# Kernel tuning notes

Hardware: AMD Instinct MI355X
Metric: run time of the kernel (lower is better)

Reference implementation:

```python
import jax, jax.numpy as jnp
import numpy as np

B, T, F = 8192, 50, 24
H1, LAT, H3 = 64, 32, 64  # encoder LSTM1, bottleneck LSTM2, decoder LSTM3


def lstm(x, W, U, b, return_sequences):
    """Keras LSTM with activation='relu', recurrent_activation='sigmoid'.
    x: [B, T, D]; W: [D, 4H]; U: [H, 4H]; b: [4H]. Gate order: i, f, g(c), o.
    """
    H = U.shape[0]
    xW = jnp.einsum('btd,dh->bth', x, W) + b          # precompute input projections
    xW_t = jnp.swapaxes(xW, 0, 1)                     # [T, B, 4H]
    h0 = jnp.zeros((x.shape[0], H), x.dtype)
    c0 = jnp.zeros((x.shape[0], H), x.dtype)

    def step(carry, xt):
        h, c = carry
        z = xt + h @ U                                 # [B, 4H]
        i = jax.nn.sigmoid(z[:, 0 * H:1 * H])
        f = jax.nn.sigmoid(z[:, 1 * H:2 * H])
        g = jax.nn.relu(z[:, 2 * H:3 * H])             # activation='relu'
        o = jax.nn.sigmoid(z[:, 3 * H:4 * H])
        c_new = f * c + i * g
        h_new = o * jax.nn.relu(c_new)                 # activation='relu'
        return (h_new, c_new), h_new

    (h_T, _), hs = jax.lax.scan(step, (h0, c0), xW_t)
    if return_sequences:
        return jnp.swapaxes(hs, 0, 1)                  # [B, T, H]
    return h_T                                         # [B, H]


def setup_inputs() -> dict:
    key = jax.random.key(0)
    ks = jax.random.split(key, 12)
    s = 0.05
    return {
        'x':  jax.random.normal(ks[0], (B, T, F), jnp.float32),
        'W1': jax.random.normal(ks[1], (F, 4 * H1), jnp.float32) * s,
        'U1': jax.random.normal(ks[2], (H1, 4 * H1), jnp.float32) * s,
        'b1': jnp.zeros((4 * H1,), jnp.float32),
        'W2': jax.random.normal(ks[3], (H1, 4 * LAT), jnp.float32) * s,
        'U2': jax.random.normal(ks[4], (LAT, 4 * LAT), jnp.float32) * s,
        'b2': jnp.zeros((4 * LAT,), jnp.float32),
        'W3': jax.random.normal(ks[5], (LAT, 4 * H3), jnp.float32) * s,
        'U3': jax.random.normal(ks[6], (H3, 4 * H3), jnp.float32) * s,
        'b3': jnp.zeros((4 * H3,), jnp.float32),
        'Wd': jax.random.normal(ks[7], (H3, F), jnp.float32) * s,
        'bd': jnp.zeros((F,), jnp.float32),
    }


def reference(x, W1, U1, b1, W2, U2, b2, W3, U3, b3, Wd, bd):
    # Encoder
    h1 = lstm(x, W1, U1, b1, return_sequences=True)    # [B, T, 64]
    z = lstm(h1, W2, U2, b2, return_sequences=False)   # [B, latent]
    # Decoder
    zr = jnp.broadcast_to(z[:, None, :], (z.shape[0], T, z.shape[1]))  # RepeatVector
    h3 = lstm(zr, W3, U3, b3, return_sequences=True)   # [B, T, 64]
    out = jnp.einsum('bth,hf->btf', h3, Wd) + bd       # TimeDistributed Dense
    return out
```

## Files before the change

### kernel.cpp

```cpp
#include <hip/hip_runtime.h>
#include <cstdint>

#define BB 8192
#define TT 50
#define FF 24
#define ROWS 32
#define LOG2E 1.4426950408889634f

typedef __attribute__((ext_vector_type(8))) short short8;
typedef __attribute__((ext_vector_type(4))) float f32x4;

__device__ __forceinline__ float sig2(float xs){
  return __builtin_amdgcn_rcpf(1.0f + exp2f(-xs));
}

__device__ __forceinline__ unsigned short rne16(float v){
  unsigned b = __float_as_uint(v);
  b += 0x7FFFu + ((b >> 16) & 1u);
  return (unsigned short)(b >> 16);
}

__device__ __forceinline__ unsigned pack2(float a, float b){
  unsigned ua = __float_as_uint(a); ua += 0x7FFFu + ((ua >> 16) & 1u);
  unsigned ub = __float_as_uint(b); ub += 0x7FFFu + ((ub >> 16) & 1u);
  return (ua >> 16) | (ub & 0xFFFF0000u);
}

__device__ __forceinline__ void phase_barrier(){
  __builtin_amdgcn_sched_barrier(0);
  asm volatile("s_waitcnt lgkmcnt(0)" ::: "memory");
  __builtin_amdgcn_s_barrier();
  asm volatile("" ::: "memory");
  __builtin_amdgcn_sched_barrier(0);
}

#define MFMA(A,B,C) __builtin_amdgcn_mfma_f32_16x16x32_bf16((A),(B),(C),0,0,0)


__global__ __launch_bounds__(1024,4)
void ae_fused(
    const float* __restrict__ x,
    const float* __restrict__ W1, const float* __restrict__ U1, const float* __restrict__ b1,
    const float* __restrict__ W2, const float* __restrict__ U2, const float* __restrict__ b2,
    const float* __restrict__ W3, const float* __restrict__ U3, const float* __restrict__ b3,
    const float* __restrict__ Wd, const float* __restrict__ bd,
    float* __restrict__ out)
{
  constexpr int AS1 = 104, AS2 = 40, AS3 = 72;
  __shared__ __align__(16) unsigned short a1[2][ROWS*AS1];
  __shared__ __align__(16) unsigned short a2[2][ROWS*AS2];
  __shared__ __align__(16) unsigned short a3[2][ROWS*AS3];

  const int tid = threadIdx.x, wave = tid>>6, lane = tid&63;
  const int quad = lane>>4, li = lane&15;
  const int w7 = wave&7, rg = wave>>3;
  const int b0 = blockIdx.x*ROWS;
  const int arow = rg*16 + li;

  const int gl = li & 3;
  const float scl = (gl==2) ? 1.0f : LOG2E;

  short8 A1w[2][3];
  f32x4 bi1[2];
#pragma unroll
  for (int tp=0; tp<2; ++tp){
    const int zc = gl*64 + 8*w7 + 2*(li>>2) + tp;
#pragma unroll
    for (int ks=0; ks<3; ++ks){
      short8 v1;
#pragma unroll
      for (int j=0; j<8; ++j){
        const int kk = quad*8 + j;
        float w;
        if (ks < 2) w = U1[(ks*32+kk)*256+zc];
        else        w = (kk<24) ? W1[kk*256+zc] : 0.f;
        v1[j] = (short)rne16(w*scl);
      }
      A1w[tp][ks]=v1;
    }
#pragma unroll
    for (int i2=0;i2<4;++i2)
      bi1[tp][i2] = b1[i2*64 + 8*w7 + 2*quad + tp] * ((i2==2)?1.0f:LOG2E);
  }
  short8 A1w2[3];
  f32x4 bi2;
  {
    const int zc = gl*32 + 4*w7 + (li>>2);
#pragma unroll
    for (int ks=0; ks<3; ++ks){
      short8 v1;
#pragma unroll
      for (int j=0; j<8; ++j){
        const int kk = quad*8 + j;
        float w = (ks<2) ? W2[(ks*32+kk)*128+zc] : U2[kk*128+zc];
        v1[j] = (short)rne16(w*scl);
      }
      A1w2[ks]=v1;
    }
#pragma unroll
    for (int i2=0;i2<4;++i2)
      bi2[i2] = b2[i2*32 + 4*w7 + quad] * ((i2==2)?1.0f:LOG2E);
  }

  { unsigned* p1 = (unsigned*)a1; for (int i=tid;i<2*ROWS*AS1/2;i+=1024) p1[i]=0u;
    unsigned* p2 = (unsigned*)a2; for (int i=tid;i<2*ROWS*AS2/2;i+=1024) p2[i]=0u;
    unsigned* p3 = (unsigned*)a3; for (int i=tid;i<2*ROWS*AS3/2;i+=1024) p3[i]=0u; }
  __syncthreads();
  if (tid < ROWS*FF){
    const int r = tid/FF, f = tid - r*FF;
    a1[0][r*AS1 + 64 + f] = rne16(x[((size_t)(b0+r)*TT + 0)*FF + f]);
  }
  int pr=0, pf=0; const float* xp=nullptr;
  float va=0.f, vb=0.f;
  const bool st = (tid < ROWS*FF);
  if (st){
    pr = tid/FF; pf = tid - pr*FF;
    xp = x + (size_t)(b0+pr)*TT*FF + pf;
    va = xp[1*FF];
    vb = xp[2*FF];
  }
  float c1s[2] = {0.f,0.f};
  float c2s = 0.f;
  const int rb1 = arow*AS1;
  const int rb2 = arow*AS2;
  const int hw1p = rb1 + 8*w7 + 2*quad;
  const int hw2 = rb2 + 4*w7 + quad;
  __syncthreads();

#pragma unroll 1
  for (int t=0; t<=TT; ++t){
    const int s = t&1, ns = s^1;
    float vc = 0.f;
    if (st && t+3 < TT) vc = xp[(t+3)*FF];
    short8 Bh0 = *(const short8*)&a1[s][rb1 +      quad*8];
    short8 Bh1 = *(const short8*)&a1[s][rb1 + 32 + quad*8];
    if (t < TT){
      short8 Bx = *(const short8*)&a1[s][rb1 + 64 + quad*8];
      float hp[2];
#pragma unroll
      for (int tp=0; tp<2; ++tp){
        f32x4 C = bi1[tp];
        C = MFMA(A1w[tp][0], Bh0, C);
        C = MFMA(A1w[tp][1], Bh1, C);
        C = MFMA(A1w[tp][2], Bx,  C);
        const float ig = sig2(C[0]), fg = sig2(C[1]);
        const float gg = fmaxf(C[2],0.f), og = sig2(C[3]);
        const float cn = fg*c1s[tp] + ig*gg; c1s[tp] = cn;
        hp[tp] = og*fmaxf(cn,0.f);
      }
      *(unsigned*)&a1[ns][hw1p] = pack2(hp[0], hp[1]);
    }
    if (t >= 1){
      f32x4 C = bi2;
      C = MFMA(A1w2[0], Bh0, C);
      C = MFMA(A1w2[1], Bh1, C);
      {
        short8 Bh2 = *(const short8*)&a2[s][rb2 + quad*8];
        C = MFMA(A1w2[2], Bh2, C);
      }
      const float ig = sig2(C[0]), fg = sig2(C[1]);
      const float gg = fmaxf(C[2],0.f), og = sig2(C[3]);
      const float cn = fg*c2s + ig*gg; c2s = cn;
      const float h = og*fmaxf(cn,0.f);
      a2[ns][hw2] = rne16(h);
    }
    if (st && t < TT-1){
      a1[ns][pr*AS1 + 64 + pf] = rne16(va);
      va = vb; vb = vc;
    }
    phase_barrier();
  }

  short8 A1u[2][2];
  short8 A1w3[2];
  f32x4 bi3[2];
#pragma unroll
  for (int tp=0; tp<2; ++tp){
    const int zc = gl*64 + 8*w7 + 2*(li>>2) + tp;
#pragma unroll
    for (int ks=0; ks<2; ++ks){
      short8 v1;
#pragma unroll
      for (int j=0; j<8; ++j){
        const int k = ks*32 + quad*8 + j;
        v1[j] = (short)rne16(U3[k*256+zc]*scl);
      }
      A1u[tp][ks]=v1;
    }
    {
      short8 v1;
#pragma unroll
      for (int j=0; j<8; ++j){
        const int k = quad*8 + j;
        v1[j] = (short)rne16(W3[k*256+zc]*scl);
      }
      A1w3[tp]=v1;
    }
#pragma unroll
    for (int i2=0;i2<4;++i2)
      bi3[tp][i2] = b3[i2*64 + 8*w7 + 2*quad + tp] * ((i2==2)?1.0f:LOG2E);
  }
  const bool dW = (w7 < 2);
  const int dcol = w7*16 + li;
  const bool dOK = dW && (dcol < 24);
  const float bdv = dOK ? bd[dcol] : 0.f;
  short8 Bd1[2];
  if (dW){
#pragma unroll
    for (int ks=0; ks<2; ++ks){
      short8 v1;
#pragma unroll
      for (int j=0; j<8; ++j){
        const int k = ks*32 + quad*8 + j;
        v1[j] = (short)rne16(dOK ? Wd[k*24+dcol] : 0.f);
      }
      Bd1[ks]=v1;
    }
  }

  f32x4 zr[2];
  {
    short8 Ba = *(const short8*)&a2[1][rb2 + quad*8];
#pragma unroll
    for (int tp=0; tp<2; ++tp){
      f32x4 C = bi3[tp];
      C = MFMA(A1w3[tp], Ba, C);
      zr[tp] = C;
    }
  }
  float c3s[2] = {0.f,0.f};
  const int rb3 = arow*AS3;
  const int hw3p = rb3 + 8*w7 + 2*quad;

#pragma unroll 1
  for (int t=0; t<=TT; ++t){
    const int s = t&1, ns = s^1;
    if (t < TT){
      short8 Ba[2];
#pragma unroll
      for (int ks=0; ks<2; ++ks)
        Ba[ks] = *(const short8*)&a3[s][rb3 + ks*32 + quad*8];
      float hp[2];
#pragma unroll
      for (int tp=0; tp<2; ++tp){
        f32x4 C = zr[tp];
        C = MFMA(A1u[tp][0], Ba[0], C);
        C = MFMA(A1u[tp][1], Ba[1], C);
        const float ig = sig2(C[0]), fg = sig2(C[1]);
        const float gg = fmaxf(C[2],0.f), og = sig2(C[3]);
        const float cn = fg*c3s[tp] + ig*gg; c3s[tp] = cn;
        hp[tp] = og*fmaxf(cn,0.f);
      }
      *(unsigned*)&a3[ns][hw3p] = pack2(hp[0], hp[1]);
      if (dW && t > 0){
        f32x4 Cd = {bdv,bdv,bdv,bdv};
        Cd = MFMA(Ba[0], Bd1[0], Cd);
        Cd = MFMA(Ba[1], Bd1[1], Cd);
        if (dcol < 24){
#pragma unroll
          for (int i2=0;i2<4;++i2)
            out[((size_t)(b0+rg*16+quad*4+i2)*TT + (t-1))*FF + dcol] = Cd[i2];
        }
      }
    } else {
      if (dW){
        f32x4 Cd = {bdv,bdv,bdv,bdv};
#pragma unroll
        for (int ks=0; ks<2; ++ks){
          short8 Ba = *(const short8*)&a3[s][rb3 + ks*32 + quad*8];
          Cd = MFMA(Ba, Bd1[ks], Cd);
        }
        if (dcol < 24){
#pragma unroll
          for (int i2=0;i2<4;++i2)
            out[((size_t)(b0+rg*16+quad*4+i2)*TT + (TT-1))*FF + dcol] = Cd[i2];
        }
      }
    }
    phase_barrier();
  }
}

extern "C" void kernel_launch(void* const* d_in, const int* in_sizes, int n_in,
                              void* d_out, int out_size, void* d_ws, size_t ws_size,
                              hipStream_t stream){
  const float* x  = (const float*)d_in[0];
  const float* W1 = (const float*)d_in[1];
  const float* U1 = (const float*)d_in[2];
  const float* b1 = (const float*)d_in[3];
  const float* W2 = (const float*)d_in[4];
  const float* U2 = (const float*)d_in[5];
  const float* b2 = (const float*)d_in[6];
  const float* W3 = (const float*)d_in[7];
  const float* U3 = (const float*)d_in[8];
  const float* b3 = (const float*)d_in[9];
  const float* Wd = (const float*)d_in[10];
  const float* bd = (const float*)d_in[11];
  float* out = (float*)d_out;

  hipLaunchKernelGGL(ae_fused, dim3(BB/ROWS), dim3(1024), 0, stream,
                     x, W1, U1, b1, W2, U2, b2, W3, U3, b3, Wd, bd, out);
}
```

Before: 219.9 us.

## Halve rows per block and spread gate columns across all sixteen waves

Each block now handles 16 batch rows instead of 32. The 16 waves each own one gate-column tile for layers 1 and 3 instead of two, and only waves 8-15 compute the layer-2 LSTM. The goal is a shorter per-step serial chain per wave (half the MFMAs and activations) and twice as many blocks, with launch bounds raised to 8 blocks per CU. The cost is half the rows per weight load, idle waves on layer 2, and higher register and occupancy pressure.

```diff
diff --git a/kernel.cpp b/kernel.cpp
--- a/kernel.cpp
+++ b/kernel.cpp
@@ -4,7 +4,7 @@
 #define BB 8192
 #define TT 50
 #define FF 24
-#define ROWS 32
+#define ROWS 16
 #define LOG2E 1.4426950408889634f
 
 typedef __attribute__((ext_vector_type(8))) short short8;
@@ -18,12 +18,6 @@
   unsigned b = __float_as_uint(v);
   b += 0x7FFFu + ((b >> 16) & 1u);
   return (unsigned short)(b >> 16);
-}
-
-__device__ __forceinline__ unsigned pack2(float a, float b){
-  unsigned ua = __float_as_uint(a); ua += 0x7FFFu + ((ua >> 16) & 1u);
-  unsigned ub = __float_as_uint(b); ub += 0x7FFFu + ((ub >> 16) & 1u);
-  return (ua >> 16) | (ub & 0xFFFF0000u);
 }
 
 __device__ __forceinline__ void phase_barrier(){
@@ -37,7 +31,7 @@
 #define MFMA(A,B,C) __builtin_amdgcn_mfma_f32_16x16x32_bf16((A),(B),(C),0,0,0)
 
 
-__global__ __launch_bounds__(1024,4)
+__global__ __launch_bounds__(1024,8)
 void ae_fused(
     const float* __restrict__ x,
     const float* __restrict__ W1, const float* __restrict__ U1, const float* __restrict__ b1,
@@ -53,18 +47,15 @@
 
   const int tid = threadIdx.x, wave = tid>>6, lane = tid&63;
   const int quad = lane>>4, li = lane&15;
-  const int w7 = wave&7, rg = wave>>3;
   const int b0 = blockIdx.x*ROWS;
-  const int arow = rg*16 + li;
 
   const int gl = li & 3;
   const float scl = (gl==2) ? 1.0f : LOG2E;
 
-  short8 A1w[2][3];
-  f32x4 bi1[2];
-#pragma unroll
-  for (int tp=0; tp<2; ++tp){
-    const int zc = gl*64 + 8*w7 + 2*(li>>2) + tp;
+  short8 A1w[3];
+  f32x4 bi1;
+  {
+    const int zc = gl*64 + 4*wave + (li>>2);
 #pragma unroll
     for (int ks=0; ks<3; ++ks){
       short8 v1;
@@ -76,15 +67,17 @@
         else        w = (kk<24) ? W1[kk*256+zc] : 0.f;
         v1[j] = (short)rne16(w*scl);
       }
-      A1w[tp][ks]=v1;
+      A1w[ks]=v1;
     }
 #pragma unroll
     for (int i2=0;i2<4;++i2)
-      bi1[tp][i2] = b1[i2*64 + 8*w7 + 2*quad + tp] * ((i2==2)?1.0f:LOG2E);
-  }
+      bi1[i2] = b1[i2*64 + 4*wave + quad] * ((i2==2)?1.0f:LOG2E);
+  }
+  const bool hasL2 = (wave >= 8);
+  const int w7 = wave & 7;
   short8 A1w2[3];
   f32x4 bi2;
-  {
+  if (hasL2){
     const int zc = gl*32 + 4*w7 + (li>>2);
 #pragma unroll
     for (int ks=0; ks<3; ++ks){
@@ -119,11 +112,11 @@
     va = xp[1*FF];
     vb = xp[2*FF];
   }
-  float c1s[2] = {0.f,0.f};
+  float c1s = 0.f;
   float c2s = 0.f;
-  const int rb1 = arow*AS1;
-  const int rb2 = arow*AS2;
-  const int hw1p = rb1 + 8*w7 + 2*quad;
+  const int rb1 = li*AS1;
+  const int rb2 = li*AS2;
+  const int hw1 = rb1 + 4*wave + quad;
   const int hw2 = rb2 + 4*w7 + quad;
   __syncthreads();
 
@@ -136,21 +129,16 @@
     short8 Bh1 = *(const short8*)&a1[s][rb1 + 32 + quad*8];
     if (t < TT){
       short8 Bx = *(const short8*)&a1[s][rb1 + 64 + quad*8];
-      float hp[2];
-#pragma unroll
-      for (int tp=0; tp<2; ++tp){
-        f32x4 C = bi1[tp];
-        C = MFMA(A1w[tp][0], Bh0, C);
-        C = MFMA(A1w[tp][1], Bh1, C);
-        C = MFMA(A1w[tp][2], Bx,  C);
-        const float ig = sig2(C[0]), fg = sig2(C[1]);
-        const float gg = fmaxf(C[2],0.f), og = sig2(C[3]);
-        const float cn = fg*c1s[tp] + ig*gg; c1s[tp] = cn;
-        hp[tp] = og*fmaxf(cn,0.f);
-      }
-      *(unsigned*)&a1[ns][hw1p] = pack2(hp[0], hp[1]);
-    }
-    if (t >= 1){
+      f32x4 C = bi1;
+      C = MFMA(A1w[0], Bh0, C);
+      C = MFMA(A1w[1], Bh1, C);
+      C = MFMA(A1w[2], Bx,  C);
+      const float ig = sig2(C[0]), fg = sig2(C[1]);
+      const float gg = fmaxf(C[2],0.f), og = sig2(C[3]);
+      const float cn = fg*c1s + ig*gg; c1s = cn;
+      a1[ns][hw1] = rne16(og*fmaxf(cn,0.f));
+    }
+    if (hasL2 && t >= 1){
       f32x4 C = bi2;
       C = MFMA(A1w2[0], Bh0, C);
       C = MFMA(A1w2[1], Bh1, C);
@@ -161,8 +149,7 @@
       const float ig = sig2(C[0]), fg = sig2(C[1]);
       const float gg = fmaxf(C[2],0.f), og = sig2(C[3]);
       const float cn = fg*c2s + ig*gg; c2s = cn;
-      const float h = og*fmaxf(cn,0.f);
-      a2[ns][hw2] = rne16(h);
+      a2[ns][hw2] = rne16(og*fmaxf(cn,0.f));
     }
     if (st && t < TT-1){
       a1[ns][pr*AS1 + 64 + pf] = rne16(va);
@@ -171,12 +158,11 @@
     phase_barrier();
   }
 
-  short8 A1u[2][2];
-  short8 A1w3[2];
-  f32x4 bi3[2];
-#pragma unroll
-  for (int tp=0; tp<2; ++tp){
-    const int zc = gl*64 + 8*w7 + 2*(li>>2) + tp;
+  short8 A1u[2];
+  short8 A1w3;
+  f32x4 bi3;
+  {
+    const int zc = gl*64 + 4*wave + (li>>2);
 #pragma unroll
     for (int ks=0; ks<2; ++ks){
       short8 v1;
@@ -185,7 +171,7 @@
         const int k = ks*32 + quad*8 + j;
         v1[j] = (short)rne16(U3[k*256+zc]*scl);
       }
-      A1u[tp][ks]=v1;
+      A1u[ks]=v1;
     }
     {
       short8 v1;
@@ -194,14 +180,14 @@
         const int k = quad*8 + j;
         v1[j] = (short)rne16(W3[k*256+zc]*scl);
       }
-      A1w3[tp]=v1;
+      A1w3=v1;
     }
 #pragma unroll
     for (int i2=0;i2<4;++i2)
-      bi3[tp][i2] = b3[i2*64 + 8*w7 + 2*quad + tp] * ((i2==2)?1.0f:LOG2E);
-  }
-  const bool dW = (w7 < 2);
-  const int dcol = w7*16 + li;
+      bi3[i2] = b3[i2*64 + 4*wave + quad] * ((i2==2)?1.0f:LOG2E);
+  }
+  const bool dW = (wave < 2);
+  const int dcol = wave*16 + li;
   const bool dOK = dW && (dcol < 24);
   const float bdv = dOK ? bd[dcol] : 0.f;
   short8 Bd1[2];
@@ -218,62 +204,51 @@
     }
   }
 
-  f32x4 zr[2];
+  f32x4 zr;
   {
     short8 Ba = *(const short8*)&a2[1][rb2 + quad*8];
-#pragma unroll
-    for (int tp=0; tp<2; ++tp){
-      f32x4 C = bi3[tp];
-      C = MFMA(A1w3[tp], Ba, C);
-      zr[tp] = C;
-    }
-  }
-  float c3s[2] = {0.f,0.f};
-  const int rb3 = arow*AS3;
-  const int hw3p = rb3 + 8*w7 + 2*quad;
+    f32x4 C = bi3;
+    C = MFMA(A1w3, Ba, C);
+    zr = C;
+  }
+  float c3s = 0.f;
+  const int rb3 = li*AS3;
+  const int hw3 = rb3 + 4*wave + quad;
 
 #pragma unroll 1
   for (int t=0; t<=TT; ++t){
     const int s = t&1, ns = s^1;
     if (t < TT){
-      short8 Ba[2];
-#pragma unroll
-      for (int ks=0; ks<2; ++ks)
-        Ba[ks] = *(const short8*)&a3[s][rb3 + ks*32 + quad*8];
-      float hp[2];
-#pragma unroll
-      for (int tp=0; tp<2; ++tp){
-        f32x4 C = zr[tp];
-        C = MFMA(A1u[tp][0], Ba[0], C);
-        C = MFMA(A1u[tp][1], Ba[1], C);
-        const float ig = sig2(C[0]), fg = sig2(C[1]);
-        const float gg = fmaxf(C[2],0.f), og = sig2(C[3]);
-        const float cn = fg*c3s[tp] + ig*gg; c3s[tp] = cn;
-        hp[tp] = og*fmaxf(cn,0.f);
-      }
-      *(unsigned*)&a3[ns][hw3p] = pack2(hp[0], hp[1]);
+      short8 Ba0 = *(const short8*)&a3[s][rb3 +      quad*8];
+      short8 Ba1 = *(const short8*)&a3[s][rb3 + 32 + quad*8];
+      f32x4 C = zr;
+      C = MFMA(A1u[0], Ba0, C);
+      C = MFMA(A1u[1], Ba1, C);
+      const float ig = sig2(C[0]), fg = sig2(C[1]);
+      const float gg = fmaxf(C[2],0.f), og = sig2(C[3]);
+      const float cn = fg*c3s + ig*gg; c3s = cn;
+      a3[ns][hw3] = rne16(og*fmaxf(cn,0.f));
       if (dW && t > 0){
         f32x4 Cd = {bdv,bdv,bdv,bdv};
-        Cd = MFMA(Ba[0], Bd1[0], Cd);
-        Cd = MFMA(Ba[1], Bd1[1], Cd);
+        Cd = MFMA(Ba0, Bd1[0], Cd);
+        Cd = MFMA(Ba1, Bd1[1], Cd);
         if (dcol < 24){
 #pragma unroll
           for (int i2=0;i2<4;++i2)
-            out[((size_t)(b0+rg*16+quad*4+i2)*TT + (t-1))*FF + dcol] = Cd[i2];
+            out[((size_t)(b0+quad*4+i2)*TT + (t-1))*FF + dcol] = Cd[i2];
         }
       }
     } else {
       if (dW){
         f32x4 Cd = {bdv,bdv,bdv,bdv};
-#pragma unroll
-        for (int ks=0; ks<2; ++ks){
-          short8 Ba = *(const short8*)&a3[s][rb3 + ks*32 + quad*8];
-          Cd = MFMA(Ba, Bd1[ks], Cd);
-        }
+        short8 Ba0 = *(const short8*)&a3[s][rb3 +      quad*8];
+        short8 Ba1 = *(const short8*)&a3[s][rb3 + 32 + quad*8];
+        Cd = MFMA(Ba0, Bd1[0], Cd);
+        Cd = MFMA(Ba1, Bd1[1], Cd);
         if (dcol < 24){
 #pragma unroll
           for (int i2=0;i2<4;++i2)
-            out[((size_t)(b0+rg*16+quad*4+i2)*TT + (TT-1))*FF + dcol] = Cd[i2];
+            out[((size_t)(b0+quad*4+i2)*TT + (TT-1))*FF + dcol] = Cd[i2];
         }
       }
     }
```

New measurement: 252.7 us. 1.15x slower.
